# Kernel tuning notes

Measured on AMD Instinct MI355X. Metric: run time of the kernel, lower is better.

The kernel has to match this reference:

```python
import jax, jax.numpy as jnp
import numpy as np
import math

DIM = 1024
WINDOW = 16
NUM_HEADS = 16
HEAD_DIM = DIM // NUM_HEADS
SCALE = math.sqrt(HEAD_DIM)
LN_EPS = 1e-5


def _gather_window(z, W):
    # z: [B, T, H, C] -> [B, T, H, W, C]; nb[:, t, :, w, :] = z[:, t-1-w] (zeros if t-1-w < 0)
    B, T, H, C = z.shape
    t = jnp.arange(T)[:, None]
    w = jnp.arange(W)[None, :]
    idx = t - 1 - w                      # [T, W]
    valid = idx >= 0
    idxc = jnp.clip(idx, 0, T - 1)
    nb = z[:, idxc]                      # [B, T, W, H, C]
    nb = jnp.where(valid[None, :, :, None, None], nb, jnp.zeros((), z.dtype))
    return nb.transpose(0, 1, 3, 2, 4)   # [B, T, H, W, C]


def setup_inputs() -> dict:
    key = jax.random.key(0)
    k0, k1, k2, k3 = jax.random.split(key, 4)
    B, T, D = 2, 4096, DIM
    x = jax.random.normal(k0, (B, T, D), dtype=jnp.float32)
    wq = jax.random.normal(k1, (D, D), dtype=jnp.float32) * 0.02
    wkv = jax.random.normal(k2, (2 * D, D), dtype=jnp.float32) * 0.02  # torch Linear weight layout [out,in]
    wo = jax.random.normal(k3, (D, D), dtype=jnp.float32) * 0.02
    gamma = jnp.ones((D,), dtype=jnp.float32)
    beta = jnp.zeros((D,), dtype=jnp.float32)
    return {"x": x, "wq": wq, "wkv": wkv, "wo": wo, "gamma": gamma, "beta": beta}


def reference(x, wq, wkv, wo, gamma, beta):
    B, T, D = x.shape
    H, HD, W = NUM_HEADS, HEAD_DIM, WINDOW
    q = (x @ wq.T).reshape(B, T, H, HD)
    kv = (x @ wkv.T).reshape(B, T, H, 2 * HD)
    nb_kv = _gather_window(kv, W)                    # [B, T, H, W, 2*HD]
    nb_k, nb_v = nb_kv[..., :HD], nb_kv[..., HD:]
    tau = jax.nn.sigmoid(jnp.einsum('bthd,bthwd->bthw', q, nb_k) / SCALE)
    msg = jnp.einsum('bthw,bthwd->bthd', tau, nb_v)  # [B, T, H, HD]
    y = x + msg.reshape(B, T, D) @ wo.T
    mu = jnp.mean(y, axis=-1, keepdims=True)
    var = jnp.mean((y - mu) ** 2, axis=-1, keepdims=True)
    out = (y - mu) * jax.lax.rsqrt(var + LN_EPS) * gamma + beta
    return out
```

## Files before the change

kernel.cpp:

```cpp
#include <hip/hip_runtime.h>
#include <hip/hip_bf16.h>

#define D_MODEL 1024
#define SEQ_T   4096
#define NBATCH  2
#define NHEADS  16
#define HEAD_D  64
#define WIN     16

typedef __attribute__((ext_vector_type(8))) short bf16x8;
typedef __attribute__((ext_vector_type(8))) unsigned short u16x8;
typedef __attribute__((ext_vector_type(4))) float f32x4;

__device__ __forceinline__ unsigned short f2bf(float f) {
  union { float f; unsigned int u; } v; v.f = f;
  unsigned int r = v.u + 0x7fffu + ((v.u >> 16) & 1u);
  return (unsigned short)(r >> 16);
}
__device__ __forceinline__ float bf2f(unsigned short u) {
  union { unsigned int u; float f; } v; v.u = ((unsigned int)u) << 16;
  return v.f;
}

#define SBAR() __builtin_amdgcn_s_barrier()
#define LGKM0() asm volatile("s_waitcnt lgkmcnt(0)" ::: "memory")
#define LGKM8() asm volatile("s_waitcnt lgkmcnt(8)" ::: "memory")
#define VMC(n) asm volatile("s_waitcnt vmcnt(" #n ")" ::: "memory")

__global__ __launch_bounds__(256) void cast_all(const float4* __restrict__ x,
                                                const float4* __restrict__ wq,
                                                const float4* __restrict__ wkv,
                                                const float4* __restrict__ wo,
                                                ushort* __restrict__ xb,
                                                ushort* __restrict__ wb) {
  int i = blockIdx.x * 256 + threadIdx.x;
  float4 v;
  ushort* dst;
  if (i < 2097152) {
    v = x[i];
    dst = xb + (size_t)i * 4;
  } else {
    int j = i - 2097152;
    const float4* src;
    int off;
    if (j < 262144) { src = wq; off = 0; }
    else if (j < 786432) { src = wkv; off = 262144; }
    else { src = wo; off = 786432; }
    v = src[j - off];
    dst = wb + (size_t)j * 4;
  }
  ushort4 o;
  o.x = f2bf(v.x); o.y = f2bf(v.y); o.z = f2bf(v.z); o.w = f2bf(v.w);
  *(ushort4*)dst = o;
}

__global__ __launch_bounds__(512, 2) void gemm1_6ph(const ushort* __restrict__ A,
                                                    const ushort* __restrict__ Bt,
                                                    ushort* __restrict__ C,
                                                    int M, int N, int K) {
  extern __shared__ char smem[];
  const int tid = threadIdx.x;
  const int wid = tid >> 6;
  const int lane = tid & 63;
  const int lin = blockIdx.y * 16 + blockIdx.x;
  const int swz = (lin & 7) * 64 + (lin >> 3);
  const int m0 = (swz >> 4) * 256;
  const int n0 = (swz & 15) * 192;

  const int l8 = lane >> 3;
  const int lchunk = (lane & 7) ^ (l8 & 7);
  const ushort* pA = A + (size_t)(m0 + wid * 8 + l8) * K + lchunk * 8;
  const ushort* pB = Bt + (size_t)(n0 + wid * 8 + l8) * K + lchunk * 8;

#define SA(kt, db, j0)                                                                     \
  {                                                                                        \
    _Pragma("unroll") for (int j = (j0); j < (j0) + 2; ++j) {                              \
      const ushort* gp = pA + (size_t)(j * 64) * K + (size_t)(kt) * 64;                    \
      char* lp = smem + (db) * 32768 + (j * 8 + wid) * 1024;                               \
      __builtin_amdgcn_global_load_lds((const __attribute__((address_space(1))) void*)gp,  \
                                       (__attribute__((address_space(3))) void*)lp, 16, 0, 0); \
    }                                                                                      \
  }
#define SB(kt, db)                                                                         \
  {                                                                                        \
    _Pragma("unroll") for (int j = 0; j < 3; ++j) {                                        \
      const ushort* gp = pB + (size_t)(j * 64) * K + (size_t)(kt) * 64;                    \
      char* lp = smem + 65536 + (db) * 24576 + (j * 8 + wid) * 1024;                       \
      __builtin_amdgcn_global_load_lds((const __attribute__((address_space(1))) void*)gp,  \
                                       (__attribute__((address_space(3))) void*)lp, 16, 0, 0); \
    }                                                                                      \
  }

  const int fr = lane & 15;
  const int g = lane >> 4;
  const int wr = wid >> 1;
  const int wc = wid & 1;
  int aRow[4], bRow[6], ch[2];
#pragma unroll
  for (int mi = 0; mi < 4; ++mi) aRow[mi] = (wr * 64 + mi * 16 + fr) * 128;
#pragma unroll
  for (int j = 0; j < 6; ++j) bRow[j] = (wc * 96 + j * 16 + fr) * 128;
#pragma unroll
  for (int kk = 0; kk < 2; ++kk) ch[kk] = ((kk * 4 + g) ^ (fr & 7)) * 16;

  f32x4 acc[4][6];
#pragma unroll
  for (int mi = 0; mi < 4; ++mi)
#pragma unroll
    for (int j = 0; j < 6; ++j) acc[mi][j] = (f32x4){0.f, 0.f, 0.f, 0.f};

  bf16x8 a[4][2], b[2][2];

#define RD_A(db)                                                               \
  _Pragma("unroll") for (int mi = 0; mi < 4; ++mi)                             \
    _Pragma("unroll") for (int kk = 0; kk < 2; ++kk)                           \
      a[mi][kk] = *(const bf16x8*)(smem + (db) * 32768 + aRow[mi] + ch[kk]);
#define RD_B(db, nh)                                                           \
  _Pragma("unroll") for (int ni = 0; ni < 2; ++ni)                             \
    _Pragma("unroll") for (int kk = 0; kk < 2; ++kk)                           \
      b[ni][kk] = *(const bf16x8*)(smem + 65536 + (db) * 24576 +               \
                                   bRow[(nh) * 2 + ni] + ch[kk]);
#define MM(nh)                                                                 \
  __builtin_amdgcn_s_setprio(1);                                               \
  _Pragma("unroll") for (int kk = 0; kk < 2; ++kk)                             \
    _Pragma("unroll") for (int mi = 0; mi < 4; ++mi)                           \
      _Pragma("unroll") for (int ni = 0; ni < 2; ++ni)                         \
        acc[mi][(nh) * 2 + ni] = __builtin_amdgcn_mfma_f32_16x16x32_bf16(      \
            a[mi][kk], b[ni][kk], acc[mi][(nh) * 2 + ni], 0, 0, 0);            \
  __builtin_amdgcn_s_setprio(0);

  SA(0, 0, 0); SA(0, 0, 2); SB(0, 0); SA(1, 1, 0); SA(1, 1, 2);
  VMC(4);
  SBAR();

#pragma unroll 1
  for (int i = 0; i < 8; ++i) {
    const int t1 = 2 * i + 1;
    const int t2 = (2 * i + 2 < 16) ? 2 * i + 2 : 15;
    const int t3 = (2 * i + 3 < 16) ? 2 * i + 3 : 15;
    const int d2 = t2 & 1, d3 = t3 & 1;

    RD_A(0); RD_B(0, 0);
    SB(t1, 1);
    LGKM8();
    SBAR(); LGKM0();
    MM(0);
    SBAR();

    RD_B(0, 1);
    SA(t2, d2, 0);
    SBAR(); LGKM0();
    MM(1);
    SBAR();

    RD_B(0, 2);
    SA(t2, d2, 2);
    VMC(4);
    SBAR(); LGKM0();
    MM(2);
    SBAR();

    RD_A(1); RD_B(1, 0);
    SB(t2, d2);
    LGKM8();
    SBAR(); LGKM0();
    MM(0);
    SBAR();

    RD_B(1, 1);
    SA(t3, d3, 0);
    SBAR(); LGKM0();
    MM(1);
    SBAR();

    RD_B(1, 2);
    SA(t3, d3, 2);
    VMC(4);
    SBAR(); LGKM0();
    MM(2);
    SBAR();
  }

  const int cc = lane & 15;
  const int cr4 = (lane >> 4) * 4;
#pragma unroll
  for (int mi = 0; mi < 4; ++mi)
#pragma unroll
    for (int j = 0; j < 6; ++j)
#pragma unroll
      for (int r = 0; r < 4; ++r) {
        int row = m0 + wr * 64 + mi * 16 + cr4 + r;
        int col = n0 + wc * 96 + j * 16 + cc;
        C[(size_t)row * N + col] = f2bf(acc[mi][j][r]);
      }
#undef SA
#undef SB
#undef RD_A
#undef RD_B
#undef MM
}

__global__ __launch_bounds__(512, 2) void gemm2_b(const ushort* __restrict__ A,
                                                  const ushort* __restrict__ Bt,
                                                  const ushort* __restrict__ residb,
                                                  ushort* __restrict__ Yb,
                                                  int M, int N, int K) {
  extern __shared__ char smem[];
  const int NTK = K >> 6;
  const int tid = threadIdx.x;
  const int wid = tid >> 6;
  const int lane = tid & 63;
  const int lin = blockIdx.y * 8 + blockIdx.x;
  const int swz = (lin & 7) * 32 + (lin >> 3);
  const int m0 = (swz >> 3) * 256;
  const int n0 = (swz & 7) * 128;

  const int l8 = lane >> 3;
  const int lchunk = (lane & 7) ^ (l8 & 7);
  const ushort* pA = A + (size_t)(m0 + wid * 8 + l8) * K + lchunk * 8;
  const ushort* pB = Bt + (size_t)(n0 + wid * 8 + l8) * K + lchunk * 8;

#define STAGE_A(kt, db)                                                                    \
  {                                                                                        \
    _Pragma("unroll") for (int j = 0; j < 4; ++j) {                                        \
      const ushort* gp = pA + (size_t)(j * 64) * K + (size_t)(kt) * 64;                    \
      char* lp = smem + (db) * 32768 + (j * 8 + wid) * 1024;                               \
      __builtin_amdgcn_global_load_lds((const __attribute__((address_space(1))) void*)gp,  \
                                       (__attribute__((address_space(3))) void*)lp, 16, 0, 0); \
    }                                                                                      \
  }
#define STAGE_B(kt, db)                                                                    \
  {                                                                                        \
    _Pragma("unroll") for (int j = 0; j < 2; ++j) {                                        \
      const ushort* gp = pB + (size_t)(j * 64) * K + (size_t)(kt) * 64;                    \
      char* lp = smem + 65536 + (db) * 16384 + (j * 8 + wid) * 1024;                       \
      __builtin_amdgcn_global_load_lds((const __attribute__((address_space(1))) void*)gp,  \
                                       (__attribute__((address_space(3))) void*)lp, 16, 0, 0); \
    }                                                                                      \
  }

  const int fr = lane & 15;
  const int g = lane >> 4;
  const int wr = wid >> 1;
  const int wc = wid & 1;
  int aRow[4], bRow[2][2], ch[2];
#pragma unroll
  for (int mi = 0; mi < 4; ++mi) aRow[mi] = (wr * 64 + mi * 16 + fr) * 128;
#pragma unroll
  for (int nq = 0; nq < 2; ++nq)
#pragma unroll
    for (int ni = 0; ni < 2; ++ni) bRow[nq][ni] = (wc * 64 + nq * 32 + ni * 16 + fr) * 128;
#pragma unroll
  for (int kk = 0; kk < 2; ++kk) ch[kk] = ((kk * 4 + g) ^ (fr & 7)) * 16;

  f32x4 acc[2][4][2];
#pragma unroll
  for (int nq = 0; nq < 2; ++nq)
#pragma unroll
    for (int mi = 0; mi < 4; ++mi)
#pragma unroll
      for (int ni = 0; ni < 2; ++ni) acc[nq][mi][ni] = (f32x4){0.f, 0.f, 0.f, 0.f};

  bf16x8 a[4][2], b0[2][2], b1[2][2];

  STAGE_A(0, 0); STAGE_B(0, 0); STAGE_A(1, 1);
  VMC(4);
  SBAR();

#define PHASE_MFMA(nq, bfr)                                                    \
  __builtin_amdgcn_s_setprio(1);                                               \
  _Pragma("unroll") for (int kk = 0; kk < 2; ++kk)                             \
    _Pragma("unroll") for (int mi = 0; mi < 4; ++mi)                           \
      _Pragma("unroll") for (int ni = 0; ni < 2; ++ni)                         \
        acc[nq][mi][ni] = __builtin_amdgcn_mfma_f32_16x16x32_bf16(             \
            a[mi][kk], bfr[ni][kk], acc[nq][mi][ni], 0, 0, 0);                 \
  __builtin_amdgcn_s_setprio(0);

#pragma unroll 1
  for (int t = 0; t < NTK; ++t) {
    const int db = t & 1;
    const int u1 = (t + 1 < NTK) ? t + 1 : NTK - 1;
    const int u2 = (t + 2 < NTK) ? t + 2 : NTK - 1;
    const int d1 = u1 & 1, d2 = u2 & 1;
    const char* Ab = smem + db * 32768;
    const char* Bb = smem + 65536 + db * 16384;

#pragma unroll
    for (int mi = 0; mi < 4; ++mi)
#pragma unroll
      for (int kk = 0; kk < 2; ++kk)
        a[mi][kk] = *(const bf16x8*)(Ab + aRow[mi] + ch[kk]);
#pragma unroll
    for (int ni = 0; ni < 2; ++ni)
#pragma unroll
      for (int kk = 0; kk < 2; ++kk)
        b0[ni][kk] = *(const bf16x8*)(Bb + bRow[0][ni] + ch[kk]);
    STAGE_B(u1, d1);
    LGKM0();
    PHASE_MFMA(0, b0);
    VMC(2);
    SBAR();

#pragma unroll
    for (int ni = 0; ni < 2; ++ni)
#pragma unroll
      for (int kk = 0; kk < 2; ++kk)
        b1[ni][kk] = *(const bf16x8*)(Bb + bRow[1][ni] + ch[kk]);
    STAGE_A(u2, d2);
    LGKM0();
    PHASE_MFMA(1, b1);
    VMC(4);
    SBAR();
  }

  const int cc = lane & 15;
  const int cr4 = (lane >> 4) * 4;
#pragma unroll
  for (int nq = 0; nq < 2; ++nq)
#pragma unroll
    for (int mi = 0; mi < 4; ++mi)
#pragma unroll
      for (int ni = 0; ni < 2; ++ni)
#pragma unroll
        for (int r = 0; r < 4; ++r) {
          int row = m0 + wr * 64 + mi * 16 + cr4 + r;
          int col = n0 + wc * 64 + nq * 32 + ni * 16 + cc;
          size_t idx = (size_t)row * N + col;
          Yb[idx] = f2bf(acc[nq][mi][ni][r] + bf2f(residb[idx]));
        }
#undef STAGE_A
#undef STAGE_B
#undef PHASE_MFMA
}

__global__ __launch_bounds__(256) void attn_win_mfma(const ushort* __restrict__ qkv,
                                                     ushort* __restrict__ msg) {
  __shared__ ushort Ks[80][72];
  __shared__ ushort Vt[64][88];
  __shared__ ushort Ps[4][16][40];

  const int tile = blockIdx.x;
  const int h = blockIdx.y;
  const int b = blockIdx.z;
  const int t0 = tile * 64;
  const size_t rowbase = (size_t)b * SEQ_T;
  const int tid = threadIdx.x;
  const int wave = tid >> 6;
  const int lane = tid & 63;

  for (int chunk = tid; chunk < 1280; chunk += 256) {
    int r = chunk >> 4;
    int c = (chunk & 15) * 8;
    int t = t0 - 16 + r;
    u16x8 u = {0, 0, 0, 0, 0, 0, 0, 0};
    if (t >= 0)
      u = *(const u16x8*)(qkv + (rowbase + t) * 3072 + 1024 + (size_t)h * 128 + c);
    if (c < 64) {
      *(u16x8*)&Ks[r][c] = u;
    } else {
      int d0 = c - 64;
#pragma unroll
      for (int j = 0; j < 8; ++j) Vt[d0 + j][r] = u[j];
    }
  }
  __syncthreads();

  const int fr = lane & 15;
  const int g = lane >> 4;
  const int rbase = wave * 16;

  bf16x8 qa[2];
#pragma unroll
  for (int kk = 0; kk < 2; ++kk)
    qa[kk] = *(const bf16x8*)(qkv + (rowbase + t0 + wave * 16 + fr) * 3072 +
                              (size_t)h * 64 + kk * 32 + g * 8);

  f32x4 sacc[2];
  sacc[0] = (f32x4){0.f, 0.f, 0.f, 0.f};
  sacc[1] = (f32x4){0.f, 0.f, 0.f, 0.f};
#pragma unroll
  for (int kk = 0; kk < 2; ++kk) {
#pragma unroll
    for (int nt = 0; nt < 2; ++nt) {
      bf16x8 kb = *(const bf16x8*)&Ks[rbase + nt * 16 + fr][kk * 32 + g * 8];
      sacc[nt] = __builtin_amdgcn_mfma_f32_16x16x32_bf16(qa[kk], kb, sacc[nt], 0, 0, 0);
    }
  }

#pragma unroll
  for (int nt = 0; nt < 2; ++nt) {
    int tk = t0 - 16 + rbase + nt * 16 + fr;
#pragma unroll
    for (int reg = 0; reg < 4; ++reg) {
      int t = t0 + wave * 16 + g * 4 + reg;
      float tau = 0.f;
      if (tk >= 0 && tk >= t - WIN && tk <= t - 1)
        tau = 1.f / (1.f + __expf(-sacc[nt][reg] * 0.125f));
      Ps[wave][g * 4 + reg][nt * 16 + fr] = f2bf(tau);
    }
  }
  __syncthreads();

  bf16x8 pa = *(const bf16x8*)&Ps[wave][fr][g * 8];
#pragma unroll
  for (int ct = 0; ct < 4; ++ct) {
    bf16x8 vb = *(const bf16x8*)&Vt[ct * 16 + fr][rbase + g * 8];
    f32x4 m = __builtin_amdgcn_mfma_f32_16x16x32_bf16(pa, vb, (f32x4){0.f, 0.f, 0.f, 0.f}, 0, 0, 0);
#pragma unroll
    for (int reg = 0; reg < 4; ++reg) {
      int t = t0 + wave * 16 + g * 4 + reg;
      msg[(rowbase + t) * 1024 + (size_t)h * 64 + ct * 16 + fr] = f2bf(m[reg]);
    }
  }
}

__global__ __launch_bounds__(256) void layernorm_b(const ushort* __restrict__ yb,
                                                   const float* __restrict__ gamma,
                                                   const float* __restrict__ beta,
                                                   float* __restrict__ out) {
  const int row = blockIdx.x;
  const ushort* p = yb + (size_t)row * D_MODEL;
  const int tid = threadIdx.x;
  ushort4 v4 = ((const ushort4*)p)[tid];
  float y0 = bf2f(v4.x), y1 = bf2f(v4.y), y2 = bf2f(v4.z), y3 = bf2f(v4.w);
  float s = y0 + y1 + y2 + y3;
  float s2 = y0 * y0 + y1 * y1 + y2 * y2 + y3 * y3;
#pragma unroll
  for (int m = 1; m < 64; m <<= 1) {
    s += __shfl_xor(s, m);
    s2 += __shfl_xor(s2, m);
  }
  __shared__ float red[8];
  const int wave = tid >> 6, lane = tid & 63;
  if (lane == 0) { red[wave] = s; red[4 + wave] = s2; }
  __syncthreads();
  s = red[0] + red[1] + red[2] + red[3];
  s2 = red[4] + red[5] + red[6] + red[7];
  const float mu = s * (1.f / D_MODEL);
  const float var = s2 * (1.f / D_MODEL) - mu * mu;
  const float rstd = rsqrtf(var + 1e-5f);
  float4 g = *(const float4*)&gamma[tid * 4];
  float4 be = *(const float4*)&beta[tid * 4];
  float4 o;
  o.x = (y0 - mu) * rstd * g.x + be.x;
  o.y = (y1 - mu) * rstd * g.y + be.y;
  o.z = (y2 - mu) * rstd * g.z + be.z;
  o.w = (y3 - mu) * rstd * g.w + be.w;
  *(float4*)&out[(size_t)row * D_MODEL + tid * 4] = o;
}

extern "C" void kernel_launch(void* const* d_in, const int* in_sizes, int n_in,
                              void* d_out, int out_size, void* d_ws, size_t ws_size,
                              hipStream_t stream) {
  (void)in_sizes; (void)n_in; (void)out_size; (void)ws_size;
  const float* x = (const float*)d_in[0];
  const float* wq = (const float*)d_in[1];
  const float* wkv = (const float*)d_in[2];
  const float* wo = (const float*)d_in[3];
  const float* gamma = (const float*)d_in[4];
  const float* beta = (const float*)d_in[5];
  float* out = (float*)d_out;

  ushort* xb = (ushort*)d_ws;
  ushort* wb = xb + (size_t)8192 * 1024;
  ushort* qkvb = wb + (size_t)4096 * 1024;
  ushort* msgb = qkvb + (size_t)8192 * 3072;
  ushort* yb = qkvb;

  const int M = NBATCH * SEQ_T;

  (void)hipFuncSetAttribute(reinterpret_cast<const void*>(&gemm1_6ph),
                            hipFuncAttributeMaxDynamicSharedMemorySize, 114688);
  (void)hipFuncSetAttribute(reinterpret_cast<const void*>(&gemm2_b),
                            hipFuncAttributeMaxDynamicSharedMemorySize, 98304);

  cast_all<<<12288, 256, 0, stream>>>((const float4*)x, (const float4*)wq,
                                      (const float4*)wkv, (const float4*)wo, xb, wb);

  gemm1_6ph<<<dim3(3072 / 192, M / 256), 512, 114688, stream>>>(xb, wb, qkvb, M, 3072, 1024);

  attn_win_mfma<<<dim3(SEQ_T / 64, NHEADS, NBATCH), 256, 0, stream>>>(qkvb, msgb);

  gemm2_b<<<dim3(1024 / 128, M / 256), 512, 98304, stream>>>(msgb, wb + (size_t)3072 * 1024,
                                                             xb, yb, M, 1024, 1024);

  layernorm_b<<<M, 256, 0, stream>>>(yb, gamma, beta, out);
}
```

Before: 120.4 us.

## Shrink QKV GEMM to 128x192 tiles with 4-wave blocks and 3-phase pipeline

The QKV projection GEMM moves from 256x192 tiles with 8 waves and 112KB of LDS to 128x192 tiles with 4 waves and 80KB of LDS. The prefetch loop is restructured from six phases per two k-tiles to three phases per k-tile. Two blocks can now fit per CU, so barriers only synchronise four waves and the grid has twice as many blocks, which should reduce the tail effect. In exchange, the smaller tile lowers A/B reuse and adds global and LDS traffic per FLOP.

Result: faster. 117.3 us (-2.6%).

```diff
diff --git a/kernel.cpp b/kernel.cpp
--- a/kernel.cpp
+++ b/kernel.cpp
@@ -54,17 +54,18 @@
   *(ushort4*)dst = o;
 }
 
-__global__ __launch_bounds__(512, 2) void gemm1_6ph(const ushort* __restrict__ A,
+__global__ __launch_bounds__(256, 2) void gemm1_2pc(const ushort* __restrict__ A,
                                                     const ushort* __restrict__ Bt,
                                                     ushort* __restrict__ C,
                                                     int M, int N, int K) {
   extern __shared__ char smem[];
+  const int NTK = K >> 6;
   const int tid = threadIdx.x;
   const int wid = tid >> 6;
   const int lane = tid & 63;
   const int lin = blockIdx.y * 16 + blockIdx.x;
-  const int swz = (lin & 7) * 64 + (lin >> 3);
-  const int m0 = (swz >> 4) * 256;
+  const int swz = (lin & 7) * 128 + (lin >> 3);
+  const int m0 = (swz >> 4) * 128;
   const int n0 = (swz & 15) * 192;
 
   const int l8 = lane >> 3;
@@ -72,20 +73,20 @@
   const ushort* pA = A + (size_t)(m0 + wid * 8 + l8) * K + lchunk * 8;
   const ushort* pB = Bt + (size_t)(n0 + wid * 8 + l8) * K + lchunk * 8;
 
-#define SA(kt, db, j0)                                                                     \
+#define SA(kt, db)                                                                         \
   {                                                                                        \
-    _Pragma("unroll") for (int j = (j0); j < (j0) + 2; ++j) {                              \
-      const ushort* gp = pA + (size_t)(j * 64) * K + (size_t)(kt) * 64;                    \
-      char* lp = smem + (db) * 32768 + (j * 8 + wid) * 1024;                               \
+    _Pragma("unroll") for (int j = 0; j < 4; ++j) {                                        \
+      const ushort* gp = pA + (size_t)(j * 32) * K + (size_t)(kt) * 64;                    \
+      char* lp = smem + (db) * 16384 + (j * 4 + wid) * 1024;                               \
       __builtin_amdgcn_global_load_lds((const __attribute__((address_space(1))) void*)gp,  \
                                        (__attribute__((address_space(3))) void*)lp, 16, 0, 0); \
     }                                                                                      \
   }
-#define SB(kt, db)                                                                         \
+#define SB(kt, db, j0)                                                                     \
   {                                                                                        \
-    _Pragma("unroll") for (int j = 0; j < 3; ++j) {                                        \
-      const ushort* gp = pB + (size_t)(j * 64) * K + (size_t)(kt) * 64;                    \
-      char* lp = smem + 65536 + (db) * 24576 + (j * 8 + wid) * 1024;                       \
+    _Pragma("unroll") for (int j = (j0); j < (j0) + 3; ++j) {                              \
+      const ushort* gp = pB + (size_t)(j * 32) * K + (size_t)(kt) * 64;                    \
+      char* lp = smem + 32768 + (db) * 24576 + (j * 4 + wid) * 1024;                       \
       __builtin_amdgcn_global_load_lds((const __attribute__((address_space(1))) void*)gp,  \
                                        (__attribute__((address_space(3))) void*)lp, 16, 0, 0); \
     }                                                                                      \
@@ -114,11 +115,11 @@
 #define RD_A(db)                                                               \
   _Pragma("unroll") for (int mi = 0; mi < 4; ++mi)                             \
     _Pragma("unroll") for (int kk = 0; kk < 2; ++kk)                           \
-      a[mi][kk] = *(const bf16x8*)(smem + (db) * 32768 + aRow[mi] + ch[kk]);
+      a[mi][kk] = *(const bf16x8*)(smem + (db) * 16384 + aRow[mi] + ch[kk]);
 #define RD_B(db, nh)                                                           \
   _Pragma("unroll") for (int ni = 0; ni < 2; ++ni)                             \
     _Pragma("unroll") for (int kk = 0; kk < 2; ++kk)                           \
-      b[ni][kk] = *(const bf16x8*)(smem + 65536 + (db) * 24576 +               \
+      b[ni][kk] = *(const bf16x8*)(smem + 32768 + (db) * 24576 +               \
                                    bRow[(nh) * 2 + ni] + ch[kk]);
 #define MM(nh)                                                                 \
   __builtin_amdgcn_s_setprio(1);                                               \
@@ -129,52 +130,32 @@
             a[mi][kk], b[ni][kk], acc[mi][(nh) * 2 + ni], 0, 0, 0);            \
   __builtin_amdgcn_s_setprio(0);
 
-  SA(0, 0, 0); SA(0, 0, 2); SB(0, 0); SA(1, 1, 0); SA(1, 1, 2);
+  SA(0, 0); SB(0, 0, 0); SB(0, 0, 3); SA(1, 1);
   VMC(4);
   SBAR();
 
 #pragma unroll 1
-  for (int i = 0; i < 8; ++i) {
-    const int t1 = 2 * i + 1;
-    const int t2 = (2 * i + 2 < 16) ? 2 * i + 2 : 15;
-    const int t3 = (2 * i + 3 < 16) ? 2 * i + 3 : 15;
-    const int d2 = t2 & 1, d3 = t3 & 1;
-
-    RD_A(0); RD_B(0, 0);
-    SB(t1, 1);
+  for (int t = 0; t < NTK; ++t) {
+    const int db = t & 1;
+    const int t1 = (t + 1 < NTK) ? t + 1 : NTK - 1;
+    const int t2 = (t + 2 < NTK) ? t + 2 : NTK - 1;
+    const int d1 = t1 & 1, d2 = t2 & 1;
+
+    RD_A(db); RD_B(db, 0);
+    SB(t1, d1, 0);
     LGKM8();
     SBAR(); LGKM0();
     MM(0);
     SBAR();
 
-    RD_B(0, 1);
-    SA(t2, d2, 0);
+    RD_B(db, 1);
+    SB(t1, d1, 3);
     SBAR(); LGKM0();
     MM(1);
     SBAR();
 
-    RD_B(0, 2);
-    SA(t2, d2, 2);
-    VMC(4);
-    SBAR(); LGKM0();
-    MM(2);
-    SBAR();
-
-    RD_A(1); RD_B(1, 0);
-    SB(t2, d2);
-    LGKM8();
-    SBAR(); LGKM0();
-    MM(0);
-    SBAR();
-
-    RD_B(1, 1);
-    SA(t3, d3, 0);
-    SBAR(); LGKM0();
-    MM(1);
-    SBAR();
-
-    RD_B(1, 2);
-    SA(t3, d3, 2);
+    RD_B(db, 2);
+    SA(t2, d2);
     VMC(4);
     SBAR(); LGKM0();
     MM(2);
@@ -469,15 +450,15 @@
 
   const int M = NBATCH * SEQ_T;
 
-  (void)hipFuncSetAttribute(reinterpret_cast<const void*>(&gemm1_6ph),
-                            hipFuncAttributeMaxDynamicSharedMemorySize, 114688);
+  (void)hipFuncSetAttribute(reinterpret_cast<const void*>(&gemm1_2pc),
+                            hipFuncAttributeMaxDynamicSharedMemorySize, 81920);
   (void)hipFuncSetAttribute(reinterpret_cast<const void*>(&gemm2_b),
                             hipFuncAttributeMaxDynamicSharedMemorySize, 98304);
 
   cast_all<<<12288, 256, 0, stream>>>((const float4*)x, (const float4*)wq,
                                       (const float4*)wkv, (const float4*)wo, xb, wb);
 
-  gemm1_6ph<<<dim3(3072 / 192, M / 256), 512, 114688, stream>>>(xb, wb, qkvb, M, 3072, 1024);
+  gemm1_2pc<<<dim3(3072 / 192, M / 128), 256, 81920, stream>>>(xb, wb, qkvb, M, 3072, 1024);
 
   attn_win_mfma<<<dim3(SEQ_T / 64, NHEADS, NBATCH), 256, 0, stream>>>(qkvb, msgb);
 
```
